# Optimization experiments

Hardware: AMD Instinct MI355X
Metric: run time of the kernel (lower is better)

The kernel has to match this reference:

```python
import jax, jax.numpy as jnp
import numpy as np

N = 8_388_608
C = 3  # 3 sentiment classes; |argmax - y| == 2 <=> class-0/class-2 confusion


def setup_inputs() -> dict:
    key = jax.random.key(0)
    k1, k2 = jax.random.split(key)
    logits = jax.random.normal(k1, (N, C), dtype=jnp.float32)
    # original module expects log-softmax outputs
    pre = jax.nn.log_softmax(logits, axis=-1)
    y_true = jax.random.randint(k2, (N,), 0, C, dtype=jnp.int64)
    weight = jnp.float32(2.0)
    return {"pre": pre, "y_true": y_true, "weight": weight}


def reference(pre, y_true, weight):
    # gather log-prob of true class: pre[i, y_true[i]]
    picked = jnp.take_along_axis(pre, y_true[:, None], axis=1)[:, 0]  # [N]
    pred = jnp.argmax(pre, axis=-1)                                   # [N]
    # penalize opposite-polarity mistakes (|pred - y| == 2)
    penal = jnp.abs(pred - y_true) == 2                               # [N] bool
    w = jnp.where(penal, weight, jnp.float32(1.0))                    # [N]
    return -jnp.sum(w * picked) / jnp.float32(pre.shape[0])
```

## Files before the change

kernel.cpp:

```cpp
#include <hip/hip_runtime.h>


#define N_ROWS   8388608
#define BLOCK    256
#define RPT      8
#define RPB      (BLOCK * RPT)
#define GRID     (N_ROWS / RPB)
#define F4PT     (RPB * 3 / 4 / BLOCK)

__global__ __launch_bounds__(BLOCK) void nll_fused_kernel(
        const float* __restrict__ pre,
        const int*   __restrict__ y_true,
        const float* __restrict__ wptr,
        float*       __restrict__ out) {
    __shared__ float tile[RPB * 3];
    __shared__ float red[BLOCK / 64];

    const float wgt = wptr[0];
    const int   t   = threadIdx.x;
    const int   rowBase = (int)blockIdx.x * RPB;
    const float4* __restrict__ pre4 = (const float4*)pre + (rowBase * 3) / 4;
    const int*    __restrict__ yb   = y_true + rowBase;

    float4 v[F4PT];
    #pragma unroll
    for (int i = 0; i < F4PT; ++i) v[i] = pre4[t + BLOCK * i];

    int yv[RPT];
    #pragma unroll
    for (int j = 0; j < RPT; ++j) yv[j] = yb[t + BLOCK * j];

    float4* tile4 = (float4*)tile;
    #pragma unroll
    for (int i = 0; i < F4PT; ++i) tile4[t + BLOCK * i] = v[i];
    __syncthreads();

    float acc = 0.0f;
    #pragma unroll
    for (int j = 0; j < RPT; ++j) {
        const int r = t + BLOCK * j;
        const float p0 = tile[3 * r + 0];
        const float p1 = tile[3 * r + 1];
        const float p2 = tile[3 * r + 2];
        const int   tt = yv[j];
        const float picked = (tt == 0) ? p0 : ((tt == 1) ? p1 : p2);
        int pred = 0;
        float m = p0;
        if (p1 > m) { m = p1; pred = 1; }
        if (p2 > m) { pred = 2; }
        const bool penal = (pred - tt == 2) || (tt - pred == 2);
        acc += (penal ? wgt : 1.0f) * picked;
    }

    #pragma unroll
    for (int off = 32; off > 0; off >>= 1)
        acc += __shfl_down(acc, off, 64);

    const int lane = t & 63;
    const int wave = t >> 6;
    if (lane == 0) red[wave] = acc;
    __syncthreads();

    if (t == 0) {
        float s = red[0] + red[1] + red[2] + red[3];
        atomicAdd(out, s * (-1.0f / (float)N_ROWS));
    }
}

extern "C" void kernel_launch(void* const* d_in, const int* in_sizes, int n_in,
                              void* d_out, int out_size, void* d_ws, size_t ws_size,
                              hipStream_t stream) {
    const float* pre  = (const float*)d_in[0];
    const int*   y    = (const int*)d_in[1];
    const float* wptr = (const float*)d_in[2];
    float* out = (float*)d_out;

    nll_fused_kernel<<<GRID, BLOCK, 0, stream>>>(pre, y, wptr, out);
}
```

Measured before the change: 187.6 us.

## Restructure to per-wave LDS tiles with double-buffered slices, removing block barrier

Each wavefront now owns its own contiguous chunk of 1024 rows, loaded as four 256-row slices into a private double-buffered LDS region. The block-wide __syncthreads before compute is replaced by an lgkmcnt wait, and the grid shrinks to 2048 blocks. The aim is to drop the block barrier and shrink the LDS footprint so occupancy and load overlap improve. In exchange it relies on intra-wave LDS visibility through an inline asm wait and has fewer blocks in flight.

```diff
diff --git a/kernel.cpp b/kernel.cpp
--- a/kernel.cpp
+++ b/kernel.cpp
@@ -3,66 +3,78 @@
 
 #define N_ROWS   8388608
 #define BLOCK    256
-#define RPT      8
-#define RPB      (BLOCK * RPT)
-#define GRID     (N_ROWS / RPB)
-#define F4PT     (RPB * 3 / 4 / BLOCK)
+#define GRID     2048
+#define WPB      (BLOCK / 64)
+#define NWAVES   (GRID * WPB)
+#define ITER     4
 
 __global__ __launch_bounds__(BLOCK) void nll_fused_kernel(
         const float* __restrict__ pre,
         const int*   __restrict__ y_true,
         const float* __restrict__ wptr,
         float*       __restrict__ out) {
-    __shared__ float tile[RPB * 3];
-    __shared__ float red[BLOCK / 64];
+    __shared__ float tile[WPB][2][768];
+    __shared__ float red[WPB];
 
-    const float wgt = wptr[0];
-    const int   t   = threadIdx.x;
-    const int   rowBase = (int)blockIdx.x * RPB;
-    const float4* __restrict__ pre4 = (const float4*)pre + (rowBase * 3) / 4;
-    const int*    __restrict__ yb   = y_true + rowBase;
+    const float wgt  = wptr[0];
+    const int   t    = threadIdx.x;
+    const int   lane = t & 63;
+    const int   wv   = t >> 6;
+    const int   W    = (int)blockIdx.x * WPB + wv;
 
-    float4 v[F4PT];
+    const float4* __restrict__ pre4 = (const float4*)pre;
+
+    float4 v[ITER][3];
+    int    yv[ITER][4];
     #pragma unroll
-    for (int i = 0; i < F4PT; ++i) v[i] = pre4[t + BLOCK * i];
-
-    int yv[RPT];
-    #pragma unroll
-    for (int j = 0; j < RPT; ++j) yv[j] = yb[t + BLOCK * j];
-
-    float4* tile4 = (float4*)tile;
-    #pragma unroll
-    for (int i = 0; i < F4PT; ++i) tile4[t + BLOCK * i] = v[i];
-    __syncthreads();
+    for (int k = 0; k < ITER; ++k) {
+        const int fb = W * (ITER * 192) + k * 192;
+        const int yb = W * (ITER * 256) + k * 256;
+        v[k][0] = pre4[fb + lane];
+        v[k][1] = pre4[fb +  64 + lane];
+        v[k][2] = pre4[fb + 128 + lane];
+        yv[k][0] = y_true[yb +        lane];
+        yv[k][1] = y_true[yb +  64  + lane];
+        yv[k][2] = y_true[yb + 128  + lane];
+        yv[k][3] = y_true[yb + 192  + lane];
+    }
 
     float acc = 0.0f;
     #pragma unroll
-    for (int j = 0; j < RPT; ++j) {
-        const int r = t + BLOCK * j;
-        const float p0 = tile[3 * r + 0];
-        const float p1 = tile[3 * r + 1];
-        const float p2 = tile[3 * r + 2];
-        const int   tt = yv[j];
-        const float picked = (tt == 0) ? p0 : ((tt == 1) ? p1 : p2);
-        int pred = 0;
-        float m = p0;
-        if (p1 > m) { m = p1; pred = 1; }
-        if (p2 > m) { pred = 2; }
-        const bool penal = (pred - tt == 2) || (tt - pred == 2);
-        acc += (penal ? wgt : 1.0f) * picked;
+    for (int k = 0; k < ITER; ++k) {
+        float*  slice = tile[wv][k & 1];
+        float4* s4    = (float4*)slice;
+        s4[lane]       = v[k][0];
+        s4[ 64 + lane] = v[k][1];
+        s4[128 + lane] = v[k][2];
+        asm volatile("s_waitcnt lgkmcnt(0)" ::: "memory");
+
+        #pragma unroll
+        for (int m = 0; m < 4; ++m) {
+            const int   w0 = 3 * lane + 192 * m;
+            const float p0 = slice[w0 + 0];
+            const float p1 = slice[w0 + 1];
+            const float p2 = slice[w0 + 2];
+            const int   tt = yv[k][m];
+            const float picked = (tt == 0) ? p0 : ((tt == 1) ? p1 : p2);
+            int   pred = 0;
+            float mx   = p0;
+            if (p1 > mx) { mx = p1; pred = 1; }
+            if (p2 > mx) { pred = 2; }
+            const bool penal = (pred - tt == 2) || (tt - pred == 2);
+            acc += (penal ? wgt : 1.0f) * picked;
+        }
     }
 
     #pragma unroll
     for (int off = 32; off > 0; off >>= 1)
         acc += __shfl_down(acc, off, 64);
 
-    const int lane = t & 63;
-    const int wave = t >> 6;
-    if (lane == 0) red[wave] = acc;
+    if (lane == 0) red[wv] = acc;
     __syncthreads();
 
     if (t == 0) {
-        float s = red[0] + red[1] + red[2] + red[3];
+        const float s = red[0] + red[1] + red[2] + red[3];
         atomicAdd(out, s * (-1.0f / (float)N_ROWS));
     }
 }
```

Measured after the change: 174.2 us. -7.2%, faster.
